# Kernel tuning notes

Measured on AMD Instinct MI355X. Metric: run time of the kernel, lower is better.

The kernel has to match this reference:

```python
import jax, jax.numpy as jnp
import numpy as np


def setup_inputs() -> dict:
    key = jax.random.key(0)
    ks = jax.random.split(key, 8)
    B, S, F, K, E, N = 20000, 10, 128, 16, 128, 200000
    nodes = jax.random.randint(ks[0], (B,), 0, N)
    neigh_idx = jax.random.randint(ks[1], (B, S), 0, N)
    self_table = jax.random.normal(ks[2], (N, F), dtype=jnp.float32)
    neigh_table = jax.random.normal(ks[3], (N, F), dtype=jnp.float32)
    center = jax.random.normal(ks[4], (K, F), dtype=jnp.float32)
    cluster_mask = jax.random.uniform(ks[5], (K, F), dtype=jnp.float32)
    # xavier-like scaling keeps exp(relu(.)) in a sane range
    weight = jax.random.normal(ks[6], (E, 2 * F), dtype=jnp.float32) * 0.05
    alpha = jax.random.normal(ks[7], (2 * F, 1), dtype=jnp.float32) * 0.05
    return {"nodes": nodes, "neigh_idx": neigh_idx, "self_table": self_table,
            "neigh_table": neigh_table, "center": center, "cluster_mask": cluster_mask,
            "weight": weight, "alpha": alpha}


def reference(nodes, neigh_idx, self_table, neigh_table, center, cluster_mask, weight, alpha):
    B, S = neigh_idx.shape
    F = self_table.shape[1]
    self_feat = self_table[nodes]                       # (B, F)
    neigh = neigh_table[neigh_idx]                      # (B, S, F) gather (== mask.matmul in original)
    # attention over sampled neighbors: exp(relu([self || neigh] @ alpha))
    a_self, a_neigh = alpha[:F, 0], alpha[F:, 0]        # split cat-matmul
    logits = self_feat @ a_self                         # (B,)
    logits = logits[:, None] + neigh @ a_neigh          # (B, S)
    att = jnp.exp(jax.nn.relu(logits))
    att_norm = att / jnp.sum(att, axis=1, keepdims=True)
    # inverse-distance soft assignment to k centers (Student-t, degree 1)
    n2 = jnp.sum(neigh * neigh, axis=-1)                # (B, S)
    c2 = jnp.sum(center * center, axis=-1)              # (K,)
    cross = jnp.einsum('bsf,kf->bsk', neigh, center)    # (B, S, K)
    q = 1.0 / (n2[:, :, None] - 2.0 * cross + c2[None, None, :] + 1.0)  # (B, S, K)
    # clustered features: sum_k q[b,s,k] * mask[k,f] * neigh[b,s,f]
    clustered = neigh * jnp.einsum('bsk,kf->bsf', q, cluster_mask)      # (B, S, F)
    neigh_agg = jnp.sum(clustered * att_norm[:, :, None], axis=1)       # (B, F)
    combined = jnp.concatenate([self_feat, neigh_agg], axis=1)          # (B, 2F)
    return jax.nn.relu(combined @ weight.T)                             # (B, E)
```

## Files before the change

### kernel.cpp

```cpp
#include <hip/hip_runtime.h>
#include <hip/hip_bf16.h>

typedef unsigned short ushort_t;
typedef __attribute__((ext_vector_type(4))) float v4f;
typedef __attribute__((ext_vector_type(8))) short v8s;

#define FDIM 128
#define KCLUST 16
#define CSTRIDE 264

__device__ __forceinline__ ushort_t f2bf(float x) {
    unsigned int u = __float_as_uint(x);
    unsigned int r = (u + 0x7fffu + ((u >> 16) & 1u)) >> 16;
    return (ushort_t)r;
}

__device__ __forceinline__ float wave_reduce_sum(float v) {
    #pragma unroll
    for (int off = 32; off > 0; off >>= 1) v += __shfl_xor(v, off, 64);
    return v;
}

__global__ void pack_weight(const float* __restrict__ W, ushort_t* __restrict__ Wb,
                            long total, long valid) {
    long i = ((long)blockIdx.x * blockDim.x + threadIdx.x) * 4;
    if (i >= total) return;
    float4 v;
    if (i < valid) v = *(const float4*)(W + i);
    else           v = make_float4(0.f, 0.f, 0.f, 0.f);
    ushort_t* dst = Wb + i;
    dst[0] = f2bf(v.x); dst[1] = f2bf(v.y); dst[2] = f2bf(v.z); dst[3] = f2bf(v.w);
}

__global__ __launch_bounds__(256) void fused_agg(
    const int* __restrict__ nodes, const int* __restrict__ neigh_idx,
    const float* __restrict__ self_table, const float* __restrict__ neigh_table,
    const float* __restrict__ center, const float* __restrict__ cluster_mask,
    const float* __restrict__ alpha, const ushort_t* __restrict__ Wb,
    float* __restrict__ out, int B, int S, int E) {

    __shared__ __align__(16) ushort_t comb[16 * CSTRIDE];
    __shared__ __align__(16) float nbuf[4 * 144];
    __shared__ __align__(16) float qbuf[4 * 16];

    int t = threadIdx.x;
    int lane = t & 63, wave = t >> 6;
    int kcl = lane & 15, blk = lane >> 4;
    int l16 = lane & 15, quad = lane >> 4;

    float as0 = alpha[lane],       as1 = alpha[lane + 64];
    float an0 = alpha[128 + lane], an1 = alpha[192 + lane];

    float cc[32];
    {
        const float* cb = center + kcl * FDIM + blk * 32;
        #pragma unroll
        for (int j = 0; j < 32; j += 4) {
            float4 v = *(const float4*)(cb + j);
            cc[j] = v.x; cc[j+1] = v.y; cc[j+2] = v.z; cc[j+3] = v.w;
        }
    }
    float mk0[KCLUST], mk1[KCLUST];
    #pragma unroll
    for (int kk = 0; kk < KCLUST; kk++) {
        mk0[kk] = cluster_mask[kk * FDIM + lane];
        mk1[kk] = cluster_mask[kk * FDIM + 64 + lane];
    }

    int b0 = blockIdx.x * 16;
    float* nb = nbuf + wave * 144;
    float* qb = qbuf + wave * 16;

    for (int r = 0; r < 4; r++) {
        int row = wave * 4 + r;
        int b = b0 + row;
        ushort_t* crow = comb + row * CSTRIDE;
        if (b >= B) {
            crow[lane] = 0; crow[lane + 64] = 0;
            crow[lane + 128] = 0; crow[lane + 192] = 0;
            continue;
        }
        size_t node = (size_t)nodes[b];
        float s0 = self_table[node * FDIM + lane];
        float s1 = self_table[node * FDIM + 64 + lane];
        float logit_self = wave_reduce_sum(s0 * as0 + s1 * as1);

        float acc0 = 0.f, acc1 = 0.f, attsum = 0.f;
        size_t g = (size_t)neigh_idx[(size_t)b * S];
        float n0 = neigh_table[g * FDIM + lane];
        float n1 = neigh_table[g * FDIM + 64 + lane];
        for (int s = 0; s < S; s++) {
            float cn0 = n0, cn1 = n1;
            if (s + 1 < S) {
                g = (size_t)neigh_idx[(size_t)b * S + s + 1];
                n0 = neigh_table[g * FDIM + lane];
                n1 = neigh_table[g * FDIM + 64 + lane];
            }
            float ln = wave_reduce_sum(cn0 * an0 + cn1 * an1);
            float att = __expf(fmaxf(logit_self + ln, 0.f));
            nb[lane + (lane >> 5) * 4] = cn0;
            int f2 = lane + 64;
            nb[f2 + (f2 >> 5) * 4] = cn1;
            float d = 0.f;
            const float* nbb = nb + blk * 36;
            #pragma unroll
            for (int i = 0; i < 8; i++) {
                float4 f4 = *(const float4*)(nbb + i * 4);
                float t0 = f4.x - cc[i*4+0]; d = fmaf(t0, t0, d);
                float t1 = f4.y - cc[i*4+1]; d = fmaf(t1, t1, d);
                float t2 = f4.z - cc[i*4+2]; d = fmaf(t2, t2, d);
                float t3 = f4.w - cc[i*4+3]; d = fmaf(t3, t3, d);
            }
            d += __shfl_xor(d, 16, 64);
            d += __shfl_xor(d, 32, 64);
            float q = 1.0f / (d + 1.0f);
            if (lane < 16) qb[lane] = q;
            float4 q0 = *(const float4*)(qb + 0);
            float4 q1 = *(const float4*)(qb + 4);
            float4 q2 = *(const float4*)(qb + 8);
            float4 q3 = *(const float4*)(qb + 12);
            float m0, m1;
            m0  = q0.x*mk0[0]  + q0.y*mk0[1]  + q0.z*mk0[2]  + q0.w*mk0[3];
            m0 += q1.x*mk0[4]  + q1.y*mk0[5]  + q1.z*mk0[6]  + q1.w*mk0[7];
            m0 += q2.x*mk0[8]  + q2.y*mk0[9]  + q2.z*mk0[10] + q2.w*mk0[11];
            m0 += q3.x*mk0[12] + q3.y*mk0[13] + q3.z*mk0[14] + q3.w*mk0[15];
            m1  = q0.x*mk1[0]  + q0.y*mk1[1]  + q0.z*mk1[2]  + q0.w*mk1[3];
            m1 += q1.x*mk1[4]  + q1.y*mk1[5]  + q1.z*mk1[6]  + q1.w*mk1[7];
            m1 += q2.x*mk1[8]  + q2.y*mk1[9]  + q2.z*mk1[10] + q2.w*mk1[11];
            m1 += q3.x*mk1[12] + q3.y*mk1[13] + q3.z*mk1[14] + q3.w*mk1[15];
            acc0 += att * cn0 * m0;
            acc1 += att * cn1 * m1;
            attsum += att;
        }
        float inv = 1.0f / attsum;
        crow[lane]       = f2bf(s0);
        crow[lane + 64]  = f2bf(s1);
        crow[lane + 128] = f2bf(acc0 * inv);
        crow[lane + 192] = f2bf(acc1 * inv);
    }
    __syncthreads();

    v8s afr[8];
    #pragma unroll
    for (int kk = 0; kk < 8; kk++)
        afr[kk] = *(const v8s*)(comb + l16 * CSTRIDE + kk * 32 + quad * 8);

    int Ntiles = (E + 15) >> 4;
    for (int nt = wave; nt < Ntiles; nt += 4) {
        const ushort_t* wrow = Wb + ((size_t)(nt * 16 + l16)) * 256 + quad * 8;
        v4f acc = {0.f, 0.f, 0.f, 0.f};
        #pragma unroll
        for (int kk = 0; kk < 8; kk++) {
            v8s bfr = *(const v8s*)(wrow + kk * 32);
            acc = __builtin_amdgcn_mfma_f32_16x16x32_bf16(afr[kk], bfr, acc, 0, 0, 0);
        }
        int gcol = nt * 16 + l16;
        if (gcol < E) {
            #pragma unroll
            for (int rr = 0; rr < 4; rr++) {
                int grow = b0 + quad * 4 + rr;
                if (grow < B)
                    out[(size_t)grow * E + gcol] = fmaxf(acc[rr], 0.f);
            }
        }
    }
}

extern "C" void kernel_launch(void* const* d_in, const int* in_sizes, int n_in,
                              void* d_out, int out_size, void* d_ws, size_t ws_size,
                              hipStream_t stream) {
    const int*   nodes        = (const int*)d_in[0];
    const int*   neigh_idx    = (const int*)d_in[1];
    const float* self_table   = (const float*)d_in[2];
    const float* neigh_table  = (const float*)d_in[3];
    const float* center       = (const float*)d_in[4];
    const float* cluster_mask = (const float*)d_in[5];
    const float* weight       = (const float*)d_in[6];
    const float* alpha        = (const float*)d_in[7];
    float* out = (float*)d_out;

    int B = in_sizes[0];
    int S = in_sizes[1] / B;
    int E = in_sizes[6] / (2 * FDIM);

    int Np = ((E + 15) / 16) * 16;
    ushort_t* Wb = (ushort_t*)d_ws;

    long totalW = (long)Np * 256;
    long validW = (long)E * 256;
    int blksW = (int)((totalW + 1023) / 1024);
    pack_weight<<<blksW, 256, 0, stream>>>(weight, Wb, totalW, validW);

    int nblk = (B + 15) / 16;
    fused_agg<<<nblk, 256, 0, stream>>>(
        nodes, neigh_idx, self_table, neigh_table, center, cluster_mask, alpha,
        Wb, out, B, S, E);
}
```

Measured before the change: 280.9 us.

## Use 512-thread blocks, two rows per wave interleaved, prefetch weight tile

Doubles block size to 8 waves so each wave handles two batch rows at once instead of four rows sequentially. The two rows' gathers, reductions and distance math are interleaved to raise memory-level parallelism. Neighbor indices are loaded once per wave and broadcast with shuffles. The first weight tile is prefetched into registers before the barrier. This adds register pressure (launch bounds 512,4) and may cause spills.

```diff
diff --git a/kernel.cpp b/kernel.cpp
--- a/kernel.cpp
+++ b/kernel.cpp
@@ -32,7 +32,7 @@
     dst[0] = f2bf(v.x); dst[1] = f2bf(v.y); dst[2] = f2bf(v.z); dst[3] = f2bf(v.w);
 }
 
-__global__ __launch_bounds__(256) void fused_agg(
+__global__ __launch_bounds__(512, 4) void fused_agg(
     const int* __restrict__ nodes, const int* __restrict__ neigh_idx,
     const float* __restrict__ self_table, const float* __restrict__ neigh_table,
     const float* __restrict__ center, const float* __restrict__ cluster_mask,
@@ -40,16 +40,15 @@
     float* __restrict__ out, int B, int S, int E) {
 
     __shared__ __align__(16) ushort_t comb[16 * CSTRIDE];
-    __shared__ __align__(16) float nbuf[4 * 144];
-    __shared__ __align__(16) float qbuf[4 * 16];
-
-    int t = threadIdx.x;
-    int lane = t & 63, wave = t >> 6;
-    int kcl = lane & 15, blk = lane >> 4;
-    int l16 = lane & 15, quad = lane >> 4;
-
-    float as0 = alpha[lane],       as1 = alpha[lane + 64];
-    float an0 = alpha[128 + lane], an1 = alpha[192 + lane];
+    __shared__ __align__(16) float nbuf[16 * 144];
+    __shared__ __align__(16) float qbuf[16 * 16];
+
+    const int t = threadIdx.x;
+    const int lane = t & 63, wave = t >> 6;
+    const int kcl = lane & 15, blk = lane >> 4;
+
+    const float as0 = alpha[lane],       as1 = alpha[lane + 64];
+    const float an0 = alpha[128 + lane], an1 = alpha[192 + lane];
 
     float cc[32];
     {
@@ -67,77 +66,158 @@
         mk1[kk] = cluster_mask[kk * FDIM + 64 + lane];
     }
 
-    int b0 = blockIdx.x * 16;
-    float* nb = nbuf + wave * 144;
-    float* qb = qbuf + wave * 16;
-
-    for (int r = 0; r < 4; r++) {
-        int row = wave * 4 + r;
-        int b = b0 + row;
-        ushort_t* crow = comb + row * CSTRIDE;
-        if (b >= B) {
-            crow[lane] = 0; crow[lane + 64] = 0;
-            crow[lane + 128] = 0; crow[lane + 192] = 0;
-            continue;
-        }
-        size_t node = (size_t)nodes[b];
-        float s0 = self_table[node * FDIM + lane];
-        float s1 = self_table[node * FDIM + 64 + lane];
-        float logit_self = wave_reduce_sum(s0 * as0 + s1 * as1);
-
-        float acc0 = 0.f, acc1 = 0.f, attsum = 0.f;
-        size_t g = (size_t)neigh_idx[(size_t)b * S];
-        float n0 = neigh_table[g * FDIM + lane];
-        float n1 = neigh_table[g * FDIM + 64 + lane];
-        for (int s = 0; s < S; s++) {
-            float cn0 = n0, cn1 = n1;
-            if (s + 1 < S) {
-                g = (size_t)neigh_idx[(size_t)b * S + s + 1];
-                n0 = neigh_table[g * FDIM + lane];
-                n1 = neigh_table[g * FDIM + 64 + lane];
-            }
-            float ln = wave_reduce_sum(cn0 * an0 + cn1 * an1);
-            float att = __expf(fmaxf(logit_self + ln, 0.f));
-            nb[lane + (lane >> 5) * 4] = cn0;
-            int f2 = lane + 64;
-            nb[f2 + (f2 >> 5) * 4] = cn1;
-            float d = 0.f;
-            const float* nbb = nb + blk * 36;
+    const int b0 = blockIdx.x * 16;
+    const int rA = wave * 2, rB = rA + 1;
+    int bA = b0 + rA, bB = b0 + rB;
+    if (bA >= B) bA = B - 1;
+    if (bB >= B) bB = B - 1;
+
+    float* const nbA = nbuf + rA * 144;
+    float* const nbB = nbuf + rB * 144;
+    float* const qbA = qbuf + rA * 16;
+    float* const qbB = qbuf + rB * 16;
+
+    float lsA, lsB;
+    {
+        size_t ndA = (size_t)nodes[bA], ndB = (size_t)nodes[bB];
+        float sA0 = self_table[ndA * FDIM + lane];
+        float sA1 = self_table[ndA * FDIM + 64 + lane];
+        float sB0 = self_table[ndB * FDIM + lane];
+        float sB1 = self_table[ndB * FDIM + 64 + lane];
+        lsA = wave_reduce_sum(sA0 * as0 + sA1 * as1);
+        lsB = wave_reduce_sum(sB0 * as0 + sB1 * as1);
+        ushort_t* crA = comb + rA * CSTRIDE;
+        ushort_t* crB = comb + rB * CSTRIDE;
+        crA[lane] = f2bf(sA0); crA[lane + 64] = f2bf(sA1);
+        crB[lane] = f2bf(sB0); crB[lane + 64] = f2bf(sB1);
+    }
+
+    int gIA = 0, gIB = 0;
+    if (lane < S) {
+        gIA = neigh_idx[(size_t)bA * S + lane];
+        gIB = neigh_idx[(size_t)bB * S + lane];
+    }
+
+    float accA0 = 0.f, accA1 = 0.f, asumA = 0.f;
+    float accB0 = 0.f, accB1 = 0.f, asumB = 0.f;
+
+    int iA = __shfl(gIA, 0, 64);
+    int iB = __shfl(gIB, 0, 64);
+    float nA0 = neigh_table[(size_t)iA * FDIM + lane];
+    float nA1 = neigh_table[(size_t)iA * FDIM + 64 + lane];
+    float nB0 = neigh_table[(size_t)iB * FDIM + lane];
+    float nB1 = neigh_table[(size_t)iB * FDIM + 64 + lane];
+
+    for (int s = 0; s < S; s++) {
+        const float cA0 = nA0, cA1 = nA1, cB0 = nB0, cB1 = nB1;
+        if (s + 1 < S) {
+            iA = __shfl(gIA, s + 1, 64);
+            iB = __shfl(gIB, s + 1, 64);
+            nA0 = neigh_table[(size_t)iA * FDIM + lane];
+            nA1 = neigh_table[(size_t)iA * FDIM + 64 + lane];
+            nB0 = neigh_table[(size_t)iB * FDIM + lane];
+            nB1 = neigh_table[(size_t)iB * FDIM + 64 + lane];
+        }
+        {
+            const int f1 = lane + (lane >> 5) * 4;
+            const int f2 = (lane + 64) + ((lane + 64) >> 5) * 4;
+            nbA[f1] = cA0; nbA[f2] = cA1;
+            nbB[f1] = cB0; nbB[f2] = cB1;
+        }
+        float lnA = cA0 * an0 + cA1 * an1;
+        float lnB = cB0 * an0 + cB1 * an1;
+        #pragma unroll
+        for (int off = 32; off > 0; off >>= 1) {
+            lnA += __shfl_xor(lnA, off, 64);
+            lnB += __shfl_xor(lnB, off, 64);
+        }
+        const float attA = __expf(fmaxf(lsA + lnA, 0.f));
+        const float attB = __expf(fmaxf(lsB + lnB, 0.f));
+
+        float dA = 0.f, dB = 0.f;
+        {
+            const float* na = nbA + blk * 36;
+            const float* nb2 = nbB + blk * 36;
             #pragma unroll
             for (int i = 0; i < 8; i++) {
-                float4 f4 = *(const float4*)(nbb + i * 4);
-                float t0 = f4.x - cc[i*4+0]; d = fmaf(t0, t0, d);
-                float t1 = f4.y - cc[i*4+1]; d = fmaf(t1, t1, d);
-                float t2 = f4.z - cc[i*4+2]; d = fmaf(t2, t2, d);
-                float t3 = f4.w - cc[i*4+3]; d = fmaf(t3, t3, d);
+                float4 a4 = *(const float4*)(na + i * 4);
+                float4 b4 = *(const float4*)(nb2 + i * 4);
+                float u;
+                u = a4.x - cc[i*4+0]; dA = fmaf(u, u, dA);
+                u = a4.y - cc[i*4+1]; dA = fmaf(u, u, dA);
+                u = a4.z - cc[i*4+2]; dA = fmaf(u, u, dA);
+                u = a4.w - cc[i*4+3]; dA = fmaf(u, u, dA);
+                u = b4.x - cc[i*4+0]; dB = fmaf(u, u, dB);
+                u = b4.y - cc[i*4+1]; dB = fmaf(u, u, dB);
+                u = b4.z - cc[i*4+2]; dB = fmaf(u, u, dB);
+                u = b4.w - cc[i*4+3]; dB = fmaf(u, u, dB);
             }
-            d += __shfl_xor(d, 16, 64);
-            d += __shfl_xor(d, 32, 64);
-            float q = 1.0f / (d + 1.0f);
-            if (lane < 16) qb[lane] = q;
-            float4 q0 = *(const float4*)(qb + 0);
-            float4 q1 = *(const float4*)(qb + 4);
-            float4 q2 = *(const float4*)(qb + 8);
-            float4 q3 = *(const float4*)(qb + 12);
-            float m0, m1;
-            m0  = q0.x*mk0[0]  + q0.y*mk0[1]  + q0.z*mk0[2]  + q0.w*mk0[3];
-            m0 += q1.x*mk0[4]  + q1.y*mk0[5]  + q1.z*mk0[6]  + q1.w*mk0[7];
-            m0 += q2.x*mk0[8]  + q2.y*mk0[9]  + q2.z*mk0[10] + q2.w*mk0[11];
-            m0 += q3.x*mk0[12] + q3.y*mk0[13] + q3.z*mk0[14] + q3.w*mk0[15];
-            m1  = q0.x*mk1[0]  + q0.y*mk1[1]  + q0.z*mk1[2]  + q0.w*mk1[3];
-            m1 += q1.x*mk1[4]  + q1.y*mk1[5]  + q1.z*mk1[6]  + q1.w*mk1[7];
-            m1 += q2.x*mk1[8]  + q2.y*mk1[9]  + q2.z*mk1[10] + q2.w*mk1[11];
-            m1 += q3.x*mk1[12] + q3.y*mk1[13] + q3.z*mk1[14] + q3.w*mk1[15];
-            acc0 += att * cn0 * m0;
-            acc1 += att * cn1 * m1;
-            attsum += att;
-        }
-        float inv = 1.0f / attsum;
-        crow[lane]       = f2bf(s0);
-        crow[lane + 64]  = f2bf(s1);
-        crow[lane + 128] = f2bf(acc0 * inv);
-        crow[lane + 192] = f2bf(acc1 * inv);
-    }
+        }
+        dA += __shfl_xor(dA, 16, 64); dA += __shfl_xor(dA, 32, 64);
+        dB += __shfl_xor(dB, 16, 64); dB += __shfl_xor(dB, 32, 64);
+        const float qA = 1.0f / (dA + 1.0f);
+        const float qB = 1.0f / (dB + 1.0f);
+        if (lane < 16) { qbA[lane] = qA; qbB[lane] = qB; }
+
+        float mA0, mA1;
+        {
+            float4 q0 = *(const float4*)(qbA + 0);
+            float4 q1 = *(const float4*)(qbA + 4);
+            float4 q2 = *(const float4*)(qbA + 8);
+            float4 q3 = *(const float4*)(qbA + 12);
+            mA0  = q0.x*mk0[0]  + q0.y*mk0[1]  + q0.z*mk0[2]  + q0.w*mk0[3];
+            mA0 += q1.x*mk0[4]  + q1.y*mk0[5]  + q1.z*mk0[6]  + q1.w*mk0[7];
+            mA0 += q2.x*mk0[8]  + q2.y*mk0[9]  + q2.z*mk0[10] + q2.w*mk0[11];
+            mA0 += q3.x*mk0[12] + q3.y*mk0[13] + q3.z*mk0[14] + q3.w*mk0[15];
+            mA1  = q0.x*mk1[0]  + q0.y*mk1[1]  + q0.z*mk1[2]  + q0.w*mk1[3];
+            mA1 += q1.x*mk1[4]  + q1.y*mk1[5]  + q1.z*mk1[6]  + q1.w*mk1[7];
+            mA1 += q2.x*mk1[8]  + q2.y*mk1[9]  + q2.z*mk1[10] + q2.w*mk1[11];
+            mA1 += q3.x*mk1[12] + q3.y*mk1[13] + q3.z*mk1[14] + q3.w*mk1[15];
+        }
+        float mB0, mB1;
+        {
+            float4 q0 = *(const float4*)(qbB + 0);
+            float4 q1 = *(const float4*)(qbB + 4);
+            float4 q2 = *(const float4*)(qbB + 8);
+            float4 q3 = *(const float4*)(qbB + 12);
+            mB0  = q0.x*mk0[0]  + q0.y*mk0[1]  + q0.z*mk0[2]  + q0.w*mk0[3];
+            mB0 += q1.x*mk0[4]  + q1.y*mk0[5]  + q1.z*mk0[6]  + q1.w*mk0[7];
+            mB0 += q2.x*mk0[8]  + q2.y*mk0[9]  + q2.z*mk0[10] + q2.w*mk0[11];
+            mB0 += q3.x*mk0[12] + q3.y*mk0[13] + q3.z*mk0[14] + q3.w*mk0[15];
+            mB1  = q0.x*mk1[0]  + q0.y*mk1[1]  + q0.z*mk1[2]  + q0.w*mk1[3];
+            mB1 += q1.x*mk1[4]  + q1.y*mk1[5]  + q1.z*mk1[6]  + q1.w*mk1[7];
+            mB1 += q2.x*mk1[8]  + q2.y*mk1[9]  + q2.z*mk1[10] + q2.w*mk1[11];
+            mB1 += q3.x*mk1[12] + q3.y*mk1[13] + q3.z*mk1[14] + q3.w*mk1[15];
+        }
+        accA0 = fmaf(attA * cA0, mA0, accA0);
+        accA1 = fmaf(attA * cA1, mA1, accA1);
+        accB0 = fmaf(attB * cB0, mB0, accB0);
+        accB1 = fmaf(attB * cB1, mB1, accB1);
+        asumA += attA; asumB += attB;
+    }
+
+    {
+        const float invA = 1.0f / asumA, invB = 1.0f / asumB;
+        ushort_t* crA = comb + rA * CSTRIDE;
+        ushort_t* crB = comb + rB * CSTRIDE;
+        crA[lane + 128] = f2bf(accA0 * invA);
+        crA[lane + 192] = f2bf(accA1 * invA);
+        crB[lane + 128] = f2bf(accB0 * invB);
+        crB[lane + 192] = f2bf(accB1 * invB);
+    }
+
+    const int l16 = lane & 15, quad = lane >> 4;
+    const int Ntiles = (E + 15) >> 4;
+
+    v8s bfr[8];
+    {
+        const int nt0 = (wave < Ntiles) ? wave : 0;
+        const ushort_t* wrow = Wb + (size_t)(nt0 * 16 + l16) * 256 + quad * 8;
+        #pragma unroll
+        for (int kk = 0; kk < 8; kk++)
+            bfr[kk] = *(const v8s*)(wrow + kk * 32);
+    }
+
     __syncthreads();
 
     v8s afr[8];
@@ -145,20 +225,22 @@
     for (int kk = 0; kk < 8; kk++)
         afr[kk] = *(const v8s*)(comb + l16 * CSTRIDE + kk * 32 + quad * 8);
 
-    int Ntiles = (E + 15) >> 4;
-    for (int nt = wave; nt < Ntiles; nt += 4) {
-        const ushort_t* wrow = Wb + ((size_t)(nt * 16 + l16)) * 256 + quad * 8;
+    for (int nt = wave; nt < Ntiles; nt += 8) {
+        if (nt != wave) {
+            const ushort_t* wrow = Wb + (size_t)(nt * 16 + l16) * 256 + quad * 8;
+            #pragma unroll
+            for (int kk = 0; kk < 8; kk++)
+                bfr[kk] = *(const v8s*)(wrow + kk * 32);
+        }
         v4f acc = {0.f, 0.f, 0.f, 0.f};
         #pragma unroll
-        for (int kk = 0; kk < 8; kk++) {
-            v8s bfr = *(const v8s*)(wrow + kk * 32);
-            acc = __builtin_amdgcn_mfma_f32_16x16x32_bf16(afr[kk], bfr, acc, 0, 0, 0);
-        }
-        int gcol = nt * 16 + l16;
+        for (int kk = 0; kk < 8; kk++)
+            acc = __builtin_amdgcn_mfma_f32_16x16x32_bf16(afr[kk], bfr[kk], acc, 0, 0, 0);
+        const int gcol = nt * 16 + l16;
         if (gcol < E) {
             #pragma unroll
             for (int rr = 0; rr < 4; rr++) {
-                int grow = b0 + quad * 4 + rr;
+                const int grow = b0 + quad * 4 + rr;
                 if (grow < B)
                     out[(size_t)grow * E + gcol] = fmaxf(acc[rr], 0.f);
             }
@@ -192,7 +274,7 @@
     pack_weight<<<blksW, 256, 0, stream>>>(weight, Wb, totalW, validW);
 
     int nblk = (B + 15) / 16;
-    fused_agg<<<nblk, 256, 0, stream>>>(
+    fused_agg<<<nblk, 512, 0, stream>>>(
         nodes, neigh_idx, self_table, neigh_table, center, cluster_mask, alpha,
         Wb, out, B, S, E);
 }
```

Measured after the change: 296.8 us. 5.7% more time.

## Restructure aggregation: 512 threads, MFMA distance and cluster-mask products

Applied to the files above, without the earlier changes.

Moves from 256 to 512 threads per block. Each row of 16 nodes is now handled by 32 threads with float4 gathers, replacing the old layout of one wave per row looped four times. The neighbor-center cross term now runs on an MFMA using bf16 operands in swizzled LDS, and the q·cluster_mask product uses three bf16 MFMAs with hi/lo splitting to keep precision. Weight tiles are also preloaded before the output GEMM. The change trades the old per-lane scalar loops for two block-wide barriers per neighbor step, adds bf16 rounding error in the distance term, and uses more LDS.

```diff
diff --git a/kernel.cpp b/kernel.cpp
--- a/kernel.cpp
+++ b/kernel.cpp
@@ -14,12 +14,11 @@
     unsigned int r = (u + 0x7fffu + ((u >> 16) & 1u)) >> 16;
     return (ushort_t)r;
 }
-
-__device__ __forceinline__ float wave_reduce_sum(float v) {
-    #pragma unroll
-    for (int off = 32; off > 0; off >>= 1) v += __shfl_xor(v, off, 64);
-    return v;
-}
+__device__ __forceinline__ float bf2f(ushort_t h) {
+    return __uint_as_float((unsigned int)h << 16);
+}
+
+union V8U { v8s v; ushort_t u[8]; };
 
 __global__ void pack_weight(const float* __restrict__ W, ushort_t* __restrict__ Wb,
                             long total, long valid) {
@@ -32,7 +31,7 @@
     dst[0] = f2bf(v.x); dst[1] = f2bf(v.y); dst[2] = f2bf(v.z); dst[3] = f2bf(v.w);
 }
 
-__global__ __launch_bounds__(256) void fused_agg(
+__global__ __launch_bounds__(512, 2) void fused_agg(
     const int* __restrict__ nodes, const int* __restrict__ neigh_idx,
     const float* __restrict__ self_table, const float* __restrict__ neigh_table,
     const float* __restrict__ center, const float* __restrict__ cluster_mask,
@@ -40,125 +39,195 @@
     float* __restrict__ out, int B, int S, int E) {
 
     __shared__ __align__(16) ushort_t comb[16 * CSTRIDE];
-    __shared__ __align__(16) float nbuf[4 * 144];
-    __shared__ __align__(16) float qbuf[4 * 16];
-
-    int t = threadIdx.x;
-    int lane = t & 63, wave = t >> 6;
-    int kcl = lane & 15, blk = lane >> 4;
-    int l16 = lane & 15, quad = lane >> 4;
-
-    float as0 = alpha[lane],       as1 = alpha[lane + 64];
-    float an0 = alpha[128 + lane], an1 = alpha[192 + lane];
-
-    float cc[32];
-    {
-        const float* cb = center + kcl * FDIM + blk * 32;
-        #pragma unroll
-        for (int j = 0; j < 32; j += 4) {
-            float4 v = *(const float4*)(cb + j);
-            cc[j] = v.x; cc[j+1] = v.y; cc[j+2] = v.z; cc[j+3] = v.w;
-        }
-    }
-    float mk0[KCLUST], mk1[KCLUST];
-    #pragma unroll
-    for (int kk = 0; kk < KCLUST; kk++) {
-        mk0[kk] = cluster_mask[kk * FDIM + lane];
-        mk1[kk] = cluster_mask[kk * FDIM + 64 + lane];
-    }
-
-    int b0 = blockIdx.x * 16;
-    float* nb = nbuf + wave * 144;
-    float* qb = qbuf + wave * 16;
-
-    for (int r = 0; r < 4; r++) {
-        int row = wave * 4 + r;
-        int b = b0 + row;
-        ushort_t* crow = comb + row * CSTRIDE;
-        if (b >= B) {
-            crow[lane] = 0; crow[lane + 64] = 0;
-            crow[lane + 128] = 0; crow[lane + 192] = 0;
-            continue;
-        }
+    __shared__ __align__(16) ushort_t nbf[2][16 * 128];
+    __shared__ __align__(16) float    nf32[2][16 * 132];
+    __shared__ __align__(16) float    attL[2][16];
+    __shared__ __align__(16) float    n2L[2][16];
+    __shared__ __align__(16) ushort_t qhi[16 * 16];
+    __shared__ __align__(16) ushort_t qlo[16 * 16];
+    __shared__ __align__(16) float    zslot[4];
+    __shared__ __align__(16) float    invL[16];
+
+    const int t    = threadIdx.x;
+    const int lane = t & 63, wave = t >> 6;
+    const int row  = t >> 5;
+    const int fq   = t & 31;
+    const int f0   = fq << 2;
+    const int l16  = lane & 15, quad = lane >> 4;
+
+    if (t < 4) zslot[t] = 0.f;
+
+    const int b0 = blockIdx.x * 16;
+    int b = b0 + row; if (b >= B) b = B - 1;
+
+    const float4 aS = *(const float4*)(alpha + f0);
+    const float4 aN = *(const float4*)(alpha + FDIM + f0);
+
+    float ls;
+    {
         size_t node = (size_t)nodes[b];
-        float s0 = self_table[node * FDIM + lane];
-        float s1 = self_table[node * FDIM + 64 + lane];
-        float logit_self = wave_reduce_sum(s0 * as0 + s1 * as1);
-
-        float acc0 = 0.f, acc1 = 0.f, attsum = 0.f;
-        size_t g = (size_t)neigh_idx[(size_t)b * S];
-        float n0 = neigh_table[g * FDIM + lane];
-        float n1 = neigh_table[g * FDIM + 64 + lane];
-        for (int s = 0; s < S; s++) {
-            float cn0 = n0, cn1 = n1;
-            if (s + 1 < S) {
-                g = (size_t)neigh_idx[(size_t)b * S + s + 1];
-                n0 = neigh_table[g * FDIM + lane];
-                n1 = neigh_table[g * FDIM + 64 + lane];
+        float4 sf = *(const float4*)(self_table + node * FDIM + f0);
+        ushort_t h0 = f2bf(sf.x), h1 = f2bf(sf.y), h2 = f2bf(sf.z), h3 = f2bf(sf.w);
+        uint2 pk;
+        pk.x = (unsigned)h0 | ((unsigned)h1 << 16);
+        pk.y = (unsigned)h2 | ((unsigned)h3 << 16);
+        *(uint2*)(comb + row * CSTRIDE + f0) = pk;
+        ls = sf.x * aS.x + sf.y * aS.y + sf.z * aS.z + sf.w * aS.w;
+        #pragma unroll
+        for (int off = 1; off <= 16; off <<= 1) ls += __shfl_xor(ls, off, 64);
+    }
+
+    v8s cbf[4]; float c2v = 0.f;
+    if (wave == 0) {
+        const float* crow = center + l16 * FDIM;
+        #pragma unroll
+        for (int kk = 0; kk < 4; kk++) {
+            const float* p = crow + kk * 32 + quad * 8;
+            float4 x = *(const float4*)p;
+            float4 y = *(const float4*)(p + 4);
+            V8U pk;
+            pk.u[0] = f2bf(x.x); pk.u[1] = f2bf(x.y); pk.u[2] = f2bf(x.z); pk.u[3] = f2bf(x.w);
+            pk.u[4] = f2bf(y.x); pk.u[5] = f2bf(y.y); pk.u[6] = f2bf(y.z); pk.u[7] = f2bf(y.w);
+            cbf[kk] = pk.v;
+            c2v += x.x*x.x + x.y*x.y + x.z*x.z + x.w*x.w
+                 + y.x*y.x + y.y*y.y + y.z*y.z + y.w*y.w;
+        }
+        c2v += __shfl_xor(c2v, 16, 64);
+        c2v += __shfl_xor(c2v, 32, 64);
+    }
+
+    v8s mhi, mlo;
+    {
+        V8U ph, pl;
+        const int fcol = wave * 16 + l16;
+        #pragma unroll
+        for (int j = 0; j < 8; j++) {
+            float mv = (quad < 2) ? cluster_mask[(quad * 8 + j) * FDIM + fcol] : 0.f;
+            ushort_t h = f2bf(mv);
+            ph.u[j] = h;
+            pl.u[j] = f2bf(mv - bf2f(h));
+        }
+        mhi = ph.v; mlo = pl.v;
+    }
+
+    int idx0 = neigh_idx[(size_t)b * S];
+    float4 n4 = *(const float4*)(neigh_table + (size_t)idx0 * FDIM + f0);
+    int idx_next = (S > 1) ? neigh_idx[(size_t)b * S + 1] : 0;
+
+    float attsum = 0.f;
+    float acc0 = 0.f, acc1 = 0.f, acc2 = 0.f, acc3 = 0.f;
+
+    for (int s = 0; s < S; s++) {
+        const int buf = s & 1;
+        const float4 cur = n4;
+        if (s + 1 < S) {
+            n4 = *(const float4*)(neigh_table + (size_t)idx_next * FDIM + f0);
+            if (s + 2 < S) idx_next = neigh_idx[(size_t)b * S + s + 2];
+        }
+
+        *(float4*)(nf32[buf] + row * 132 + f0) = cur;
+        {
+            ushort_t h0 = f2bf(cur.x), h1 = f2bf(cur.y), h2 = f2bf(cur.z), h3 = f2bf(cur.w);
+            uint2 pk;
+            pk.x = (unsigned)h0 | ((unsigned)h1 << 16);
+            pk.y = (unsigned)h2 | ((unsigned)h3 << 16);
+            const int slot = (fq >> 1) ^ (row & 15);
+            *(uint2*)((char*)(nbf[buf]) + row * 256 + slot * 16 + (fq & 1) * 8) = pk;
+        }
+        float pn = cur.x * aN.x + cur.y * aN.y + cur.z * aN.z + cur.w * aN.w;
+        float p2 = cur.x * cur.x + cur.y * cur.y + cur.z * cur.z + cur.w * cur.w;
+        #pragma unroll
+        for (int off = 1; off <= 16; off <<= 1) {
+            pn += __shfl_xor(pn, off, 64);
+            p2 += __shfl_xor(p2, off, 64);
+        }
+        const float att = __expf(fmaxf(ls + pn, 0.f));
+        attsum += att;
+        if (fq == 0) { attL[buf][row] = att; n2L[buf][row] = p2; }
+        __syncthreads();
+
+        if (wave == 0) {
+            v4f xacc = {0.f, 0.f, 0.f, 0.f};
+            #pragma unroll
+            for (int kk = 0; kk < 4; kk++) {
+                const int sl = (kk * 4 + quad) ^ l16;
+                v8s af = *(const v8s*)((char*)(nbf[buf]) + l16 * 256 + sl * 16);
+                xacc = __builtin_amdgcn_mfma_f32_16x16x32_bf16(af, cbf[kk], xacc, 0, 0, 0);
             }
-            float ln = wave_reduce_sum(cn0 * an0 + cn1 * an1);
-            float att = __expf(fmaxf(logit_self + ln, 0.f));
-            nb[lane + (lane >> 5) * 4] = cn0;
-            int f2 = lane + 64;
-            nb[f2 + (f2 >> 5) * 4] = cn1;
-            float d = 0.f;
-            const float* nbb = nb + blk * 36;
-            #pragma unroll
-            for (int i = 0; i < 8; i++) {
-                float4 f4 = *(const float4*)(nbb + i * 4);
-                float t0 = f4.x - cc[i*4+0]; d = fmaf(t0, t0, d);
-                float t1 = f4.y - cc[i*4+1]; d = fmaf(t1, t1, d);
-                float t2 = f4.z - cc[i*4+2]; d = fmaf(t2, t2, d);
-                float t3 = f4.w - cc[i*4+3]; d = fmaf(t3, t3, d);
+            const float4 n2r = *(const float4*)(&n2L[buf][quad * 4]);
+            #pragma unroll
+            for (int r = 0; r < 4; r++) {
+                const float n2v = (r == 0) ? n2r.x : (r == 1) ? n2r.y : (r == 2) ? n2r.z : n2r.w;
+                const float d  = n2v - 2.f * xacc[r] + c2v;
+                const float qv = 1.f / (d + 1.f);
+                const ushort_t h = f2bf(qv);
+                qhi[(quad * 4 + r) * 16 + l16] = h;
+                qlo[(quad * 4 + r) * 16 + l16] = f2bf(qv - bf2f(h));
             }
-            d += __shfl_xor(d, 16, 64);
-            d += __shfl_xor(d, 32, 64);
-            float q = 1.0f / (d + 1.0f);
-            if (lane < 16) qb[lane] = q;
-            float4 q0 = *(const float4*)(qb + 0);
-            float4 q1 = *(const float4*)(qb + 4);
-            float4 q2 = *(const float4*)(qb + 8);
-            float4 q3 = *(const float4*)(qb + 12);
-            float m0, m1;
-            m0  = q0.x*mk0[0]  + q0.y*mk0[1]  + q0.z*mk0[2]  + q0.w*mk0[3];
-            m0 += q1.x*mk0[4]  + q1.y*mk0[5]  + q1.z*mk0[6]  + q1.w*mk0[7];
-            m0 += q2.x*mk0[8]  + q2.y*mk0[9]  + q2.z*mk0[10] + q2.w*mk0[11];
-            m0 += q3.x*mk0[12] + q3.y*mk0[13] + q3.z*mk0[14] + q3.w*mk0[15];
-            m1  = q0.x*mk1[0]  + q0.y*mk1[1]  + q0.z*mk1[2]  + q0.w*mk1[3];
-            m1 += q1.x*mk1[4]  + q1.y*mk1[5]  + q1.z*mk1[6]  + q1.w*mk1[7];
-            m1 += q2.x*mk1[8]  + q2.y*mk1[9]  + q2.z*mk1[10] + q2.w*mk1[11];
-            m1 += q3.x*mk1[12] + q3.y*mk1[13] + q3.z*mk1[14] + q3.w*mk1[15];
-            acc0 += att * cn0 * m0;
-            acc1 += att * cn1 * m1;
-            attsum += att;
-        }
-        float inv = 1.0f / attsum;
-        crow[lane]       = f2bf(s0);
-        crow[lane + 64]  = f2bf(s1);
-        crow[lane + 128] = f2bf(acc0 * inv);
-        crow[lane + 192] = f2bf(acc1 * inv);
-    }
+        }
+        __syncthreads();
+
+        v8s aqh = (quad < 2) ? *(const v8s*)((char*)qhi + l16 * 32 + quad * 16)
+                             : *(const v8s*)zslot;
+        v8s aql = (quad < 2) ? *(const v8s*)((char*)qlo + l16 * 32 + quad * 16)
+                             : *(const v8s*)zslot;
+        v4f mac = {0.f, 0.f, 0.f, 0.f};
+        mac = __builtin_amdgcn_mfma_f32_16x16x32_bf16(aqh, mhi, mac, 0, 0, 0);
+        mac = __builtin_amdgcn_mfma_f32_16x16x32_bf16(aql, mhi, mac, 0, 0, 0);
+        mac = __builtin_amdgcn_mfma_f32_16x16x32_bf16(aqh, mlo, mac, 0, 0, 0);
+
+        const float4 attr = *(const float4*)(&attL[buf][quad * 4]);
+        const float* nfp = nf32[buf] + wave * 16 + l16;
+        acc0 = fmaf(attr.x * mac[0], nfp[(quad * 4 + 0) * 132], acc0);
+        acc1 = fmaf(attr.y * mac[1], nfp[(quad * 4 + 1) * 132], acc1);
+        acc2 = fmaf(attr.z * mac[2], nfp[(quad * 4 + 2) * 132], acc2);
+        acc3 = fmaf(attr.w * mac[3], nfp[(quad * 4 + 3) * 132], acc3);
+    }
+
+    if (fq == 0) invL[row] = 1.f / attsum;
     __syncthreads();
+    {
+        const float4 invr = *(const float4*)(&invL[quad * 4]);
+        ushort_t* cp = comb + 128 + wave * 16 + l16;
+        cp[(quad * 4 + 0) * CSTRIDE] = f2bf(acc0 * invr.x);
+        cp[(quad * 4 + 1) * CSTRIDE] = f2bf(acc1 * invr.y);
+        cp[(quad * 4 + 2) * CSTRIDE] = f2bf(acc2 * invr.z);
+        cp[(quad * 4 + 3) * CSTRIDE] = f2bf(acc3 * invr.w);
+    }
+    __syncthreads();
+
+    const int Ntiles = (E + 15) >> 4;
+
+    v8s bfr[8];
+    {
+        const int nt0 = (wave < Ntiles) ? wave : 0;
+        const ushort_t* wrow = Wb + (size_t)(nt0 * 16 + l16) * 256 + quad * 8;
+        #pragma unroll
+        for (int kk = 0; kk < 8; kk++)
+            bfr[kk] = *(const v8s*)(wrow + kk * 32);
+    }
 
     v8s afr[8];
     #pragma unroll
     for (int kk = 0; kk < 8; kk++)
         afr[kk] = *(const v8s*)(comb + l16 * CSTRIDE + kk * 32 + quad * 8);
 
-    int Ntiles = (E + 15) >> 4;
-    for (int nt = wave; nt < Ntiles; nt += 4) {
-        const ushort_t* wrow = Wb + ((size_t)(nt * 16 + l16)) * 256 + quad * 8;
+    for (int nt = wave; nt < Ntiles; nt += 8) {
+        if (nt != wave) {
+            const ushort_t* wrow = Wb + (size_t)(nt * 16 + l16) * 256 + quad * 8;
+            #pragma unroll
+            for (int kk = 0; kk < 8; kk++)
+                bfr[kk] = *(const v8s*)(wrow + kk * 32);
+        }
         v4f acc = {0.f, 0.f, 0.f, 0.f};
         #pragma unroll
-        for (int kk = 0; kk < 8; kk++) {
-            v8s bfr = *(const v8s*)(wrow + kk * 32);
-            acc = __builtin_amdgcn_mfma_f32_16x16x32_bf16(afr[kk], bfr, acc, 0, 0, 0);
-        }
-        int gcol = nt * 16 + l16;
+        for (int kk = 0; kk < 8; kk++)
+            acc = __builtin_amdgcn_mfma_f32_16x16x32_bf16(afr[kk], bfr[kk], acc, 0, 0, 0);
+        const int gcol = nt * 16 + l16;
         if (gcol < E) {
             #pragma unroll
             for (int rr = 0; rr < 4; rr++) {
-                int grow = b0 + quad * 4 + rr;
+                const int grow = b0 + quad * 4 + rr;
                 if (grow < B)
                     out[(size_t)grow * E + gcol] = fmaxf(acc[rr], 0.f);
             }
@@ -192,7 +261,7 @@
     pack_weight<<<blksW, 256, 0, stream>>>(weight, Wb, totalW, validW);
 
     int nblk = (B + 15) / 16;
-    fused_agg<<<nblk, 256, 0, stream>>>(
+    fused_agg<<<nblk, 512, 0, stream>>>(
         nodes, neigh_idx, self_table, neigh_table, center, cluster_mask, alpha,
         Wb, out, B, S, E);
 }
```

Result: faster. 233.4 us (-16.9%).
